# Optimization experiments

Measured on AMD Instinct MI355X. Metric: run time of the kernel, lower is better.

## Reference

```python
import jax, jax.numpy as jnp
import numpy as np

EMBED = 1024
HEADS = 16
HEAD_DIM = EMBED // HEADS
MLP = 4 * EMBED
EPS = 1e-6


def setup_inputs() -> dict:
    key = jax.random.key(0)
    ks = jax.random.split(key, 16)
    B, N, C = 2, 2048, EMBED
    x = jax.random.normal(ks[0], (B, N, C), dtype=jnp.float32)
    c = jax.random.normal(ks[1], (B, C), dtype=jnp.float32)
    attention_mask = jax.random.randint(ks[2], (B, N), 0, 2, dtype=jnp.int32)
    s = 0.02
    params = {
        "norm_w": jnp.ones((C,), jnp.float32),
        "scale_w": s * jax.random.normal(ks[3], (C, C), jnp.float32),
        "scale_b": s * jax.random.normal(ks[4], (C,), jnp.float32),
        "shift_w": s * jax.random.normal(ks[5], (C, C), jnp.float32),
        "shift_b": s * jax.random.normal(ks[6], (C,), jnp.float32),
        "qkv_w": s * jax.random.normal(ks[7], (3 * C, C), jnp.float32),
        "proj_w": s * jax.random.normal(ks[8], (C, C), jnp.float32),
        "proj_b": s * jax.random.normal(ks[9], (C,), jnp.float32),
        "mlp_w1": s * jax.random.normal(ks[10], (2 * MLP, C), jnp.float32),
        "mlp_b1": s * jax.random.normal(ks[11], (2 * MLP,), jnp.float32),
        "mlp_w2": s * jax.random.normal(ks[12], (C, MLP), jnp.float32),
        "mlp_b2": s * jax.random.normal(ks[13], (C,), jnp.float32),
    }
    return {"x": x, "c": c, "attention_mask": attention_mask, **params}


def _adaln(x, c, norm_w, scale_w, scale_b, shift_w, shift_b):
    sc = jax.nn.silu(c)
    shift = sc @ shift_w.T + shift_b                      # [B,C]
    scale = jnp.clip(sc @ scale_w.T + scale_b + 1.0, 0.1, 10.0)
    # RMSNorm: ||x|| * C^-0.5, clamped below by eps
    norm = jnp.maximum(jnp.linalg.norm(x, axis=-1, keepdims=True) * x.shape[-1] ** -0.5, EPS)
    h = x / norm * norm_w
    return h * scale[:, None, :] + shift[:, None, :]


def _attention(x, attention_mask, qkv_w, proj_w, proj_b):
    B, N, C = x.shape
    qkv = (x @ qkv_w.T).reshape(B, N, 3, HEADS, HEAD_DIM)
    q = qkv[:, :, 0].transpose(0, 2, 1, 3)  # [B,H,N,D]
    k = qkv[:, :, 1].transpose(0, 2, 1, 3)
    v = qkv[:, :, 2].transpose(0, 2, 1, 3)
    attn = jnp.einsum("bhnd,bhmd->bhnm", q, k) * (HEAD_DIM ** -0.5)
    mask = attention_mask[:, None, None, :]              # [B,1,1,N] over keys
    attn = jnp.where(mask == 0, -jnp.inf, attn)
    all_inf = jnp.all(attn == -jnp.inf, axis=-1, keepdims=True)
    attn = jnp.where(all_inf, 0.0, attn)
    p = jax.nn.softmax(attn, axis=-1)
    out = jnp.einsum("bhnm,bhmd->bhnd", p, v).transpose(0, 2, 1, 3).reshape(B, N, C)
    return out @ proj_w.T + proj_b


def _mlp(x, w1, b1, w2, b2):
    h = x @ w1.T + b1
    x1, x2 = jnp.split(h, 2, axis=-1)
    return (jax.nn.silu(x1) * x2) @ w2.T + b2


def reference(x, c, attention_mask, norm_w, scale_w, scale_b, shift_w, shift_b,
              qkv_w, proj_w, proj_b, mlp_w1, mlp_b1, mlp_w2, mlp_b2):
    x = x + _attention(_adaln(x, c, norm_w, scale_w, scale_b, shift_w, shift_b),
                       attention_mask, qkv_w, proj_w, proj_b)
    x = x + _mlp(_adaln(x, c, norm_w, scale_w, scale_b, shift_w, shift_b),
                 mlp_w1, mlp_b1, mlp_w2, mlp_b2)
    return x
```

## Files before the change

### kernel.cpp

```cpp
#include <hip/hip_runtime.h>
#include <cstdint>
#include <cstddef>

#define DEVINL __device__ __forceinline__

typedef __bf16 bf16x8 __attribute__((ext_vector_type(8)));
typedef float  f32x4  __attribute__((ext_vector_type(4)));


DEVINL unsigned short f2b(float f) {
  unsigned u = __builtin_bit_cast(unsigned, f);
  u += 0x7fffu + ((u >> 16) & 1u);
  return (unsigned short)(u >> 16);
}

DEVINL unsigned packtrunc(float a, float b) {
  unsigned ua = __builtin_bit_cast(unsigned, a);
  unsigned ub = __builtin_bit_cast(unsigned, b);
  return (ua >> 16) | (ub & 0xffff0000u);
}

DEVINL void async16(void* lds, const void* g) {
  __builtin_amdgcn_global_load_lds((const __attribute__((address_space(1))) unsigned*)g,
                                   (__attribute__((address_space(3))) unsigned*)lds,
                                   16, 0, 0);
}


__global__ void cvt4_kernel(const float* __restrict__ s0, const float* __restrict__ s1,
                            const float* __restrict__ s2, const float* __restrict__ s3,
                            unsigned short* __restrict__ d0, unsigned short* __restrict__ d1,
                            unsigned short* __restrict__ d2, unsigned short* __restrict__ d3) {
  int i = blockIdx.x * 256 + threadIdx.x;
  if (i < 786432) {
    float4 v = ((const float4*)s0)[i];
    ushort4 o; o.x = f2b(v.x); o.y = f2b(v.y); o.z = f2b(v.z); o.w = f2b(v.w);
    ((ushort4*)d0)[i] = o;
  } else if (i < 1048576) {
    int off = i - 786432;
    float4 v = ((const float4*)s1)[off];
    ushort4 o; o.x = f2b(v.x); o.y = f2b(v.y); o.z = f2b(v.z); o.w = f2b(v.w);
    ((ushort4*)d1)[off] = o;
  } else if (i < 3145728) {
    int off = i - 1048576;
    int row = off >> 8, col = off & 255;
    int rp = (row < 4096) ? (row << 1) : (((row - 4096) << 1) | 1);
    float4 v = ((const float4*)s2)[off];
    ushort4 o; o.x = f2b(v.x); o.y = f2b(v.y); o.z = f2b(v.z); o.w = f2b(v.w);
    ((ushort4*)d2)[rp * 256 + col] = o;
  } else {
    int off = i - 3145728;
    float4 v = ((const float4*)s3)[off];
    ushort4 o; o.x = f2b(v.x); o.y = f2b(v.y); o.z = f2b(v.z); o.w = f2b(v.w);
    ((ushort4*)d3)[off] = o;
  }
}


__global__ void cond_kernel(const float* __restrict__ c,
                            const float* __restrict__ scale_w, const float* __restrict__ scale_b,
                            const float* __restrict__ shift_w, const float* __restrict__ shift_b,
                            float* __restrict__ scale_o, float* __restrict__ shift_o) {
  __shared__ float sc[1024];
  __shared__ float red[2][4][64];
  int tid = threadIdx.x;
  int b = blockIdx.x >> 4, ch = blockIdx.x & 15;
  for (int i = tid; i < 1024; i += 256) {
    float cv = c[b * 1024 + i];
    sc[i] = cv / (1.f + __expf(-cv));
  }
  __syncthreads();
  int colidx = tid & 63, p = tid >> 6;
  int co = ch * 64 + colidx;
  float dsc = 0.f, dsh = 0.f;
  for (int i = 0; i < 256; ++i) {
    int kk = p * 256 + i;
    float s = sc[kk];
    dsc += s * scale_w[(size_t)co * 1024 + kk];
    dsh += s * shift_w[(size_t)co * 1024 + kk];
  }
  red[0][p][colidx] = dsc;
  red[1][p][colidx] = dsh;
  __syncthreads();
  if (p == 0) {
    float s4  = red[0][0][colidx] + red[0][1][colidx] + red[0][2][colidx] + red[0][3][colidx];
    float sh4 = red[1][0][colidx] + red[1][1][colidx] + red[1][2][colidx] + red[1][3][colidx];
    scale_o[b * 1024 + co] = fminf(fmaxf(s4 + scale_b[co] + 1.f, 0.1f), 10.f);
    shift_o[b * 1024 + co] = sh4 + shift_b[co];
  }
}


__global__ __launch_bounds__(256) void adaln_kernel(const float* __restrict__ x,
                                                    const float* __restrict__ norm_w,
                                                    const float* __restrict__ scale,
                                                    const float* __restrict__ shift,
                                                    unsigned short* __restrict__ h) {
  int row = blockIdx.x;
  int b = row >> 11;
  int tid = threadIdx.x;
  float4 v = ((const float4*)(x + (size_t)row * 1024))[tid];
  float ss = v.x * v.x + v.y * v.y + v.z * v.z + v.w * v.w;
  #pragma unroll
  for (int d = 32; d; d >>= 1) ss += __shfl_xor(ss, d);
  __shared__ float wsum[4];
  if ((tid & 63) == 0) wsum[tid >> 6] = ss;
  __syncthreads();
  float tot = wsum[0] + wsum[1] + wsum[2] + wsum[3];
  float inv = 1.f / fmaxf(sqrtf(tot * (1.f / 1024.f)), 1e-6f);
  float4 nw  = ((const float4*)norm_w)[tid];
  float4 scv = ((const float4*)(scale + b * 1024))[tid];
  float4 shv = ((const float4*)(shift + b * 1024))[tid];
  ushort4 o;
  o.x = f2b(v.x * inv * nw.x * scv.x + shv.x);
  o.y = f2b(v.y * inv * nw.y * scv.y + shv.y);
  o.z = f2b(v.z * inv * nw.z * scv.z + shv.z);
  o.w = f2b(v.w * inv * nw.w * scv.w + shv.w);
  ((ushort4*)(h + (size_t)row * 1024))[tid] = o;
}


template<int EPI, int MT>
__global__ __launch_bounds__(256, 1) void gemm_k(
    const unsigned short* __restrict__ A,
    const unsigned short* __restrict__ B0,
    const float* __restrict__ bias0,
    const float* __restrict__ resid,
    void* __restrict__ out0_, void* __restrict__ out1_, void* __restrict__ out2_,
    int M, int N, int K) {
  constexpr int MI = MT / 32;
  constexpr int A_SH = MT * 32;
  constexpr int COMPUTE_SH = 2 * A_SH + 2 * 4096;
  constexpr int STAGE_SH = (EPI == 1) ? 128 * 136 : (EPI == 2 ? 128 * 72 : 0);
  constexpr int SMEM_SH = (COMPUTE_SH > STAGE_SH) ? COMPUTE_SH : STAGE_SH;
  __shared__ __align__(16) unsigned short smem[SMEM_SH];
  unsigned short* As0 = smem;
  unsigned short* As1 = smem + A_SH;
  unsigned short* Bs0 = smem + 2 * A_SH;
  unsigned short* Bs1 = smem + 2 * A_SH + 4096;

  const int tid = threadIdx.x;
  const int wave = tid >> 6, lane = tid & 63;
  const int quad = lane >> 4, l16 = lane & 15;
  const int wm = (wave >> 1) * (MT / 2), wn = (wave & 1) * 64;
  const int bm = blockIdx.y * MT, bn = blockIdx.x * 128;

  f32x4 acc[MI][4] = {};

  const int steps = K >> 6;
  for (int s = 0; s < steps; ++s) {
    const int k0 = s << 6;
    __syncthreads();
    #pragma unroll
    for (int i = 0; i < MT / 64; ++i) {
      int cc = i * 256 + tid;
      int r = cc >> 2, ko = (cc & 3) << 3;
      size_t ga = (size_t)(bm + r) * K + k0 + ko;
      async16(As0 + (i * 2048 + wave * 512), A + ga);
      async16(As1 + (i * 2048 + wave * 512), A + ga + 32);
    }
    #pragma unroll
    for (int i = 0; i < 2; ++i) {
      int cc = i * 256 + tid;
      int r = cc >> 2, ko = (cc & 3) << 3;
      size_t gb = (size_t)(bn + r) * K + k0 + ko;
      async16(Bs0 + (i * 2048 + wave * 512), B0 + gb);
      async16(Bs1 + (i * 2048 + wave * 512), B0 + gb + 32);
    }
    __syncthreads();
    #pragma unroll
    for (int ks = 0; ks < 2; ++ks) {
      const unsigned short* Ah = ks ? As1 : As0;
      const unsigned short* Bh = ks ? Bs1 : Bs0;
      bf16x8 af[MI], bfr[4];
      #pragma unroll
      for (int mi = 0; mi < MI; ++mi)
        af[mi] = *reinterpret_cast<const bf16x8*>(&Ah[(wm + mi * 16 + l16) * 32 + quad * 8]);
      #pragma unroll
      for (int ni = 0; ni < 4; ++ni)
        bfr[ni] = *reinterpret_cast<const bf16x8*>(&Bh[(wn + ni * 16 + l16) * 32 + quad * 8]);
      #pragma unroll
      for (int mi = 0; mi < MI; ++mi)
        #pragma unroll
        for (int ni = 0; ni < 4; ++ni)
          acc[mi][ni] = __builtin_amdgcn_mfma_f32_16x16x32_bf16(af[mi], bfr[ni], acc[mi][ni], 0, 0, 0);
    }
  }

  if constexpr (EPI == 0) {
    #pragma unroll
    for (int mi = 0; mi < MI; ++mi) {
      #pragma unroll
      for (int ni = 0; ni < 4; ++ni) {
        int gc = bn + wn + ni * 16 + l16;
        #pragma unroll
        for (int r = 0; r < 4; ++r) {
          int gr = bm + wm + mi * 16 + quad * 4 + r;
          ((float*)out0_)[(size_t)gr * N + gc] = acc[mi][ni][r] + bias0[gc] + resid[(size_t)gr * N + gc];
        }
      }
    }
  } else if constexpr (EPI == 1) {
    const int region = bn >> 10;
    __syncthreads();
    #pragma unroll
    for (int mi = 0; mi < MI; ++mi) {
      #pragma unroll
      for (int ni = 0; ni < 4; ++ni) {
        int lc = wn + ni * 16 + l16;
        #pragma unroll
        for (int r = 0; r < 4; ++r) {
          int lr = wm + mi * 16 + quad * 4 + r;
          float v = acc[mi][ni][r];
          if (region == 0)      smem[lr * 136 + lc] = f2b(v * 0.125f);
          else if (region == 1) smem[lr * 136 + lc] = f2b(v);
          else                  smem[lc * 136 + lr] = f2b(v);
        }
      }
    }
    __syncthreads();
    const int b = bm >> 11;
    const int bnm = bn & 1023;
    if (region <= 1) {
      int lr = tid >> 1, hl = tid & 1;
      int n = (bm + lr) & 2047;
      int hh = (bnm >> 6) + hl;
      unsigned short* dst = (unsigned short*)(region == 0 ? out0_ : out1_) +
                            (((size_t)(b * 16 + hh)) * 2048 + n) * 64;
      const unsigned short* src = smem + lr * 136 + hl * 64;
      #pragma unroll
      for (int j = 0; j < 8; ++j)
        ((uint4*)dst)[j] = *(const uint4*)(src + j * 8);
    } else {
      int lc = tid >> 1, nh = tid & 1;
      int c2 = bnm + lc;
      int hh = c2 >> 6, d = c2 & 63;
      int nbase = (bm & 2047) + nh * 64;
      unsigned short* dst = (unsigned short*)out2_ +
                            (((size_t)(b * 16 + hh)) * 64 + d) * 2048 + nbase;
      const unsigned short* src = smem + lc * 136 + nh * 64;
      #pragma unroll
      for (int j = 0; j < 8; ++j)
        ((uint4*)dst)[j] = *(const uint4*)(src + j * 8);
    }
  } else {
    __syncthreads();
    #pragma unroll
    for (int mi = 0; mi < MI; ++mi) {
      #pragma unroll
      for (int ni = 0; ni < 4; ++ni) {
        int lc = wn + ni * 16 + l16;
        int gcp = bn + lc;
        int gi = gcp >> 1;
        float bias = bias0[(gcp & 1) ? 4096 + gi : gi];
        #pragma unroll
        for (int r = 0; r < 4; ++r) {
          int lr = wm + mi * 16 + quad * 4 + r;
          float v = acc[mi][ni][r] + bias;
          float p = __shfl_xor(v, 1);
          if ((l16 & 1) == 0) {
            float g = (v / (1.f + __expf(-v))) * p;
            smem[lr * 72 + (lc >> 1)] = f2b(g);
          }
        }
      }
    }
    __syncthreads();
    int lr = tid >> 1, ch = (tid & 1) * 32;
    unsigned short* dst = (unsigned short*)out0_ + (size_t)(bm + lr) * (N >> 1) + (bn >> 1) + ch;
    const unsigned short* src = smem + lr * 72 + ch;
    #pragma unroll
    for (int j = 0; j < 4; ++j)
      ((uint4*)dst)[j] = *(const uint4*)(src + j * 8);
  }
}


__global__ __launch_bounds__(512, 1) void attn_kernel(
    const unsigned short* __restrict__ q, const unsigned short* __restrict__ k,
    const unsigned short* __restrict__ vt, const int* __restrict__ amask,
    unsigned short* __restrict__ o) {
  const int bh = blockIdx.x;
  const int b = bh >> 4, h = bh & 15;
  const int qt = blockIdx.y;
  const int tid = threadIdx.x;
  const int wave = tid >> 6, lane = tid & 63;
  const int quad = lane >> 4, l16 = lane & 15;
  const int h7 = l16 & 7;
  const int kc0 = (quad ^ h7) * 8;
  const int kc1 = ((quad + 4) ^ h7) * 8;

  const unsigned short* qb = q  + (size_t)bh * 2048 * 64;
  const unsigned short* kb = k  + (size_t)bh * 2048 * 64;
  const unsigned short* vb = vt + (size_t)bh * 64 * 2048;

  __shared__ __align__(16) unsigned short Ks[64 * 64];
  __shared__ __align__(16) unsigned short Vs[64 * 64];
  __shared__ __align__(16) unsigned short Ps[8 * 16 * 72];
  __shared__ float biasf[64];

  unsigned short* PsW = Ps + wave * 1152;

  const int qrow = qt * 128 + wave * 16 + l16;
  bf16x8 qa0 = *reinterpret_cast<const bf16x8*>(&qb[(size_t)qrow * 64 + quad * 8]);
  bf16x8 qa1 = *reinterpret_cast<const bf16x8*>(&qb[(size_t)qrow * 64 + 32 + quad * 8]);

  f32x4 oacc[4] = {};
  float mrow = -30000.f, lrow = 0.f;

  uint4 kpre, vpre;
  {
    int key = tid >> 3, dl = (tid & 7) ^ (key & 7);
    kpre = *(const uint4*)(kb + key * 64 + dl * 8);
    int d = tid >> 3, kl = (tid & 7) ^ (d & 7);
    vpre = *(const uint4*)(vb + (size_t)d * 2048 + kl * 8);
  }
  int mv = (tid < 64) ? amask[b * 2048 + tid] : 0;

  for (int kt = 0; kt < 32; ++kt) {
    __syncthreads();
    ((uint4*)Ks)[tid] = kpre;
    ((uint4*)Vs)[tid] = vpre;
    if (tid < 64) biasf[tid] = mv ? 0.f : -30000.f;
    __syncthreads();

    if (kt + 1 < 32) {
      int key = tid >> 3, dl = (tid & 7) ^ (key & 7);
      kpre = *(const uint4*)(kb + (size_t)(kt + 1) * 4096 + key * 64 + dl * 8);
      int d = tid >> 3, kl = (tid & 7) ^ (d & 7);
      vpre = *(const uint4*)(vb + (size_t)d * 2048 + (kt + 1) * 64 + kl * 8);
      mv = (tid < 64) ? amask[b * 2048 + (kt + 1) * 64 + tid] : 0;
    }

    f32x4 st[4];
    #pragma unroll
    for (int nt = 0; nt < 4; ++nt) {
      bf16x8 ka0 = *reinterpret_cast<const bf16x8*>(&Ks[(nt * 16 + l16) * 64 + kc0]);
      bf16x8 ka1 = *reinterpret_cast<const bf16x8*>(&Ks[(nt * 16 + l16) * 64 + kc1]);
      f32x4 bv = *reinterpret_cast<const f32x4*>(&biasf[nt * 16 + quad * 4]);
      f32x4 z = {};
      z = __builtin_amdgcn_mfma_f32_16x16x32_bf16(ka0, qa0, z, 0, 0, 0);
      z = __builtin_amdgcn_mfma_f32_16x16x32_bf16(ka1, qa1, z, 0, 0, 0);
      st[nt] = z + bv;
    }

    float tm = -1e30f;
    #pragma unroll
    for (int nt = 0; nt < 4; ++nt)
      #pragma unroll
      for (int r = 0; r < 4; ++r) tm = fmaxf(tm, st[nt][r]);
    tm = fmaxf(tm, __shfl_xor(tm, 16));
    tm = fmaxf(tm, __shfl_xor(tm, 32));

    float mnew = fmaxf(mrow, tm);
    float alpha = __expf(mrow - mnew);
    mrow = mnew;

    float rs = 0.f;
    #pragma unroll
    for (int nt = 0; nt < 4; ++nt) {
      float p0 = __expf(st[nt][0] - mnew);
      float p1 = __expf(st[nt][1] - mnew);
      float p2 = __expf(st[nt][2] - mnew);
      float p3 = __expf(st[nt][3] - mnew);
      rs += (p0 + p1) + (p2 + p3);
      uint2 w;
      w.x = packtrunc(p0, p1);
      w.y = packtrunc(p2, p3);
      *(uint2*)&PsW[l16 * 72 + nt * 16 + quad * 4] = w;
    }
    rs += __shfl_xor(rs, 16);
    rs += __shfl_xor(rs, 32);
    lrow = lrow * alpha + rs;

    float a0 = __shfl(alpha, quad * 4 + 0);
    float a1 = __shfl(alpha, quad * 4 + 1);
    float a2 = __shfl(alpha, quad * 4 + 2);
    float a3 = __shfl(alpha, quad * 4 + 3);
    #pragma unroll
    for (int dt = 0; dt < 4; ++dt) {
      oacc[dt][0] *= a0; oacc[dt][1] *= a1; oacc[dt][2] *= a2; oacc[dt][3] *= a3;
    }

    bf16x8 pa0 = *reinterpret_cast<const bf16x8*>(&PsW[l16 * 72 + quad * 8]);
    bf16x8 pa1 = *reinterpret_cast<const bf16x8*>(&PsW[l16 * 72 + 32 + quad * 8]);
    #pragma unroll
    for (int dt = 0; dt < 4; ++dt) {
      bf16x8 vb0 = *reinterpret_cast<const bf16x8*>(&Vs[(dt * 16 + l16) * 64 + kc0]);
      bf16x8 vb1 = *reinterpret_cast<const bf16x8*>(&Vs[(dt * 16 + l16) * 64 + kc1]);
      oacc[dt] = __builtin_amdgcn_mfma_f32_16x16x32_bf16(pa0, vb0, oacc[dt], 0, 0, 0);
      oacc[dt] = __builtin_amdgcn_mfma_f32_16x16x32_bf16(pa1, vb1, oacc[dt], 0, 0, 0);
    }
  }

  float invl = lrow > 0.f ? 1.f / lrow : 0.f;
  float i0 = __shfl(invl, quad * 4 + 0);
  float i1 = __shfl(invl, quad * 4 + 1);
  float i2 = __shfl(invl, quad * 4 + 2);
  float i3 = __shfl(invl, quad * 4 + 3);
  __syncthreads();
  #pragma unroll
  for (int dt = 0; dt < 4; ++dt) {
    int lr = wave * 16 + quad * 4;
    Ps[(lr + 0) * 72 + dt * 16 + l16] = f2b(oacc[dt][0] * i0);
    Ps[(lr + 1) * 72 + dt * 16 + l16] = f2b(oacc[dt][1] * i1);
    Ps[(lr + 2) * 72 + dt * 16 + l16] = f2b(oacc[dt][2] * i2);
    Ps[(lr + 3) * 72 + dt * 16 + l16] = f2b(oacc[dt][3] * i3);
  }
  __syncthreads();
  {
    int lr = tid >> 2, cb = (tid & 3) * 16;
    int n = qt * 128 + lr;
    unsigned short* dst = o + ((size_t)(b * 2048 + n)) * 1024 + h * 64 + cb;
    const unsigned short* src = Ps + lr * 72 + cb;
    ((uint4*)dst)[0] = *(const uint4*)(src);
    ((uint4*)dst)[1] = *(const uint4*)(src + 8);
  }
}


extern "C" void kernel_launch(void* const* d_in, const int* in_sizes, int n_in,
                              void* d_out, int out_size, void* d_ws, size_t ws_size,
                              hipStream_t stream) {
  const float* x       = (const float*)d_in[0];
  const float* c       = (const float*)d_in[1];
  const int*   amask   = (const int*)d_in[2];
  const float* norm_w  = (const float*)d_in[3];
  const float* scale_w = (const float*)d_in[4];
  const float* scale_b = (const float*)d_in[5];
  const float* shift_w = (const float*)d_in[6];
  const float* shift_b = (const float*)d_in[7];
  const float* qkv_w   = (const float*)d_in[8];
  const float* proj_w  = (const float*)d_in[9];
  const float* proj_b  = (const float*)d_in[10];
  const float* mlp_w1  = (const float*)d_in[11];
  const float* mlp_b1  = (const float*)d_in[12];
  const float* mlp_w2  = (const float*)d_in[13];
  const float* mlp_b2  = (const float*)d_in[14];

  char* ws = (char*)d_ws;
  unsigned short* wqkv  = (unsigned short*)(ws + 0);
  unsigned short* wproj = (unsigned short*)(ws + 6291456);
  unsigned short* wmlp1 = (unsigned short*)(ws + 8388608);
  unsigned short* wmlp2 = (unsigned short*)(ws + 25165824);
  float* scale_o        = (float*)(ws + 33554432);
  float* shift_o        = (float*)(ws + 33562624);
  unsigned short* hbuf  = (unsigned short*)(ws + 33570816);
  unsigned short* qbuf  = (unsigned short*)(ws + 41959424);
  unsigned short* kbuf  = (unsigned short*)(ws + 50348032);
  unsigned short* vbuf  = (unsigned short*)(ws + 58736640);
  unsigned short* abuf  = (unsigned short*)(ws + 67125248);
  unsigned short* gbuf  = qbuf;
  float* x1             = (float*)(ws + 75513856);

  cvt4_kernel<<<16384, 256, 0, stream>>>(qkv_w, proj_w, mlp_w1, mlp_w2,
                                         wqkv, wproj, wmlp1, wmlp2);

  cond_kernel<<<32, 256, 0, stream>>>(c, scale_w, scale_b, shift_w, shift_b, scale_o, shift_o);

  adaln_kernel<<<4096, 256, 0, stream>>>(x, norm_w, scale_o, shift_o, hbuf);

  gemm_k<1, 128><<<dim3(24, 32), 256, 0, stream>>>(hbuf, wqkv, nullptr, nullptr,
                                                   qbuf, kbuf, vbuf, 4096, 3072, 1024);

  attn_kernel<<<dim3(32, 16), 512, 0, stream>>>(qbuf, kbuf, vbuf, amask, abuf);

  gemm_k<0, 64><<<dim3(8, 64), 256, 0, stream>>>(abuf, wproj, proj_b, x,
                                                 x1, nullptr, nullptr, 4096, 1024, 1024);

  adaln_kernel<<<4096, 256, 0, stream>>>(x1, norm_w, scale_o, shift_o, hbuf);

  gemm_k<2, 128><<<dim3(64, 32), 256, 0, stream>>>(hbuf, wmlp1, mlp_b1, nullptr,
                                                   gbuf, nullptr, nullptr, 4096, 8192, 1024);

  gemm_k<0, 64><<<dim3(8, 64), 256, 0, stream>>>(gbuf, wmlp2, mlp_b2, x1,
                                                 d_out, nullptr, nullptr, 4096, 1024, 4096);

  (void)in_sizes; (void)n_in; (void)out_size; (void)ws_size;
}
```

Before: 468.0 us.

## Add 256x256-tile GLU GEMM kernel for MLP up-projection

```diff
diff --git a/kernel.cpp b/kernel.cpp
--- a/kernel.cpp
+++ b/kernel.cpp
@@ -276,6 +276,129 @@
 }
 
 
+__global__ __launch_bounds__(512, 2) void gemm256_glu(
+    const unsigned short* __restrict__ A,
+    const unsigned short* __restrict__ B,
+    const float* __restrict__ bias,
+    unsigned short* __restrict__ out,
+    int M, int N, int K) {
+  __shared__ __align__(16) unsigned short smem[65536];
+
+  const int tid  = threadIdx.x;
+  const int wave = tid >> 6, lane = tid & 63;
+  const int quad = lane >> 4, l16 = lane & 15;
+  const int wm = (wave >> 2) * 128, wn = (wave & 3) * 64;
+
+  const int nwg = gridDim.x * gridDim.y;
+  int lin = blockIdx.y * gridDim.x + blockIdx.x;
+  int cpx = nwg >> 3;
+  int swz = (lin & 7) * cpx + (lin >> 3);
+  int bx = swz % gridDim.x, by = swz / gridDim.x;
+  const int bm = by * 256, bn = bx * 256;
+
+  const unsigned short* gA[4];
+  const unsigned short* gB[4];
+  #pragma unroll
+  for (int j = 0; j < 4; ++j) {
+    int cc = j * 512 + tid;
+    int r  = cc >> 3;
+    int lc = (cc & 7) ^ (r & 7);
+    gA[j] = A + (size_t)(bm + r) * K + lc * 8;
+    gB[j] = B + (size_t)(bn + r) * K + lc * 8;
+  }
+
+  f32x4 acc[8][4] = {};
+  const int T = K >> 6;
+
+  #pragma unroll
+  for (int j = 0; j < 4; ++j) async16(smem +         j * 4096 + wave * 512, gA[j]);
+  #pragma unroll
+  for (int j = 0; j < 4; ++j) async16(smem + 32768 + j * 4096 + wave * 512, gB[j]);
+  #pragma unroll
+  for (int j = 0; j < 4; ++j) async16(smem + 16384 + j * 4096 + wave * 512, gA[j] + 64);
+  #pragma unroll
+  for (int j = 0; j < 4; ++j) async16(smem + 49152 + j * 4096 + wave * 512, gB[j] + 64);
+  asm volatile("s_waitcnt vmcnt(8)" ::: "memory");
+  __builtin_amdgcn_s_barrier();
+
+  const int pc0 = quad ^ (l16 & 7);
+  const int pc1 = (quad + 4) ^ (l16 & 7);
+
+  for (int t = 0; t < T; ++t) {
+    const int cur = t & 1;
+    const unsigned short* As = smem + cur * 16384;
+    const unsigned short* Bs = smem + 32768 + cur * 16384;
+
+    bf16x8 bfr[4][2];
+    #pragma unroll
+    for (int ni = 0; ni < 4; ++ni) {
+      int rb = (wn + ni * 16 + l16) * 64;
+      bfr[ni][0] = *reinterpret_cast<const bf16x8*>(&Bs[rb + pc0 * 8]);
+      bfr[ni][1] = *reinterpret_cast<const bf16x8*>(&Bs[rb + pc1 * 8]);
+    }
+    __builtin_amdgcn_s_setprio(1);
+    #pragma unroll
+    for (int mi = 0; mi < 8; ++mi) {
+      int ra = (wm + mi * 16 + l16) * 64;
+      bf16x8 a0 = *reinterpret_cast<const bf16x8*>(&As[ra + pc0 * 8]);
+      bf16x8 a1 = *reinterpret_cast<const bf16x8*>(&As[ra + pc1 * 8]);
+      #pragma unroll
+      for (int ni = 0; ni < 4; ++ni)
+        acc[mi][ni] = __builtin_amdgcn_mfma_f32_16x16x32_bf16(a0, bfr[ni][0], acc[mi][ni], 0, 0, 0);
+      #pragma unroll
+      for (int ni = 0; ni < 4; ++ni)
+        acc[mi][ni] = __builtin_amdgcn_mfma_f32_16x16x32_bf16(a1, bfr[ni][1], acc[mi][ni], 0, 0, 0);
+    }
+    __builtin_amdgcn_s_setprio(0);
+
+    asm volatile("s_waitcnt lgkmcnt(0)" ::: "memory");
+    __builtin_amdgcn_s_barrier();
+
+    if (t + 2 < T) {
+      const int ko = (t + 2) << 6;
+      #pragma unroll
+      for (int j = 0; j < 4; ++j) async16(smem + cur * 16384 +         j * 4096 + wave * 512, gA[j] + ko);
+      #pragma unroll
+      for (int j = 0; j < 4; ++j) async16(smem + cur * 16384 + 32768 + j * 4096 + wave * 512, gB[j] + ko);
+      asm volatile("s_waitcnt vmcnt(8)" ::: "memory");
+      __builtin_amdgcn_s_barrier();
+    } else if (t + 1 < T) {
+      asm volatile("s_waitcnt vmcnt(0)" ::: "memory");
+      __builtin_amdgcn_s_barrier();
+    }
+  }
+
+  #pragma unroll
+  for (int ni = 0; ni < 4; ++ni) {
+    int lc = wn + ni * 16 + l16;
+    int gi = (bn + lc) >> 1;
+    float bv = bias[(l16 & 1) ? 4096 + gi : gi];
+    #pragma unroll
+    for (int mi = 0; mi < 8; ++mi) {
+      #pragma unroll
+      for (int r = 0; r < 4; ++r) {
+        float v = acc[mi][ni][r] + bv;
+        float p = __shfl_xor(v, 1);
+        if ((l16 & 1) == 0) {
+          int lr = wm + mi * 16 + quad * 4 + r;
+          float g = (v / (1.f + __expf(-v))) * p;
+          smem[lr * 136 + (lc >> 1)] = f2b(g);
+        }
+      }
+    }
+  }
+  __syncthreads();
+  {
+    int lr = tid >> 1, half = (tid & 1) * 64;
+    unsigned short* dst = out + (size_t)(bm + lr) * (N >> 1) + (bn >> 1) + half;
+    const unsigned short* src = smem + lr * 136 + half;
+    #pragma unroll
+    for (int j = 0; j < 8; ++j)
+      ((uint4*)dst)[j] = *(const uint4*)(src + j * 8);
+  }
+}
+
+
 __global__ __launch_bounds__(512, 1) void attn_kernel(
     const unsigned short* __restrict__ q, const unsigned short* __restrict__ k,
     const unsigned short* __restrict__ vt, const int* __restrict__ amask,
@@ -470,8 +593,7 @@
 
   adaln_kernel<<<4096, 256, 0, stream>>>(x1, norm_w, scale_o, shift_o, hbuf);
 
-  gemm_k<2, 128><<<dim3(64, 32), 256, 0, stream>>>(hbuf, wmlp1, mlp_b1, nullptr,
-                                                   gbuf, nullptr, nullptr, 4096, 8192, 1024);
+  gemm256_glu<<<dim3(32, 16), 512, 0, stream>>>(hbuf, wmlp1, mlp_b1, gbuf, 4096, 8192, 1024);
 
   gemm_k<0, 64><<<dim3(8, 64), 256, 0, stream>>>(gbuf, wmlp2, mlp_b2, x1,
                                                  d_out, nullptr, nullptr, 4096, 1024, 4096);
```

New measurement: 482.2 us. 3.0% more time.

## Add 256x256-tile 8-wave GEMM with fused SwiGLU epilogue for MLP up-projection

Applied to the files above, without the earlier changes.

```diff
diff --git a/kernel.cpp b/kernel.cpp
--- a/kernel.cpp
+++ b/kernel.cpp
@@ -276,6 +276,153 @@
 }
 
 
+__global__ __launch_bounds__(512, 2) void gemm256_glu(
+    const unsigned short* __restrict__ A,
+    const unsigned short* __restrict__ B,
+    const float* __restrict__ bias,
+    unsigned short* __restrict__ out,
+    int M, int N, int K) {
+  __shared__ __align__(16) unsigned short smem[65536];
+
+  const int tid  = threadIdx.x;
+  const int wave = tid >> 6, lane = tid & 63;
+  const int quad = lane >> 4, l16 = lane & 15;
+  const int wm = (wave >> 2) * 128, wn = (wave & 3) * 64;
+
+  const int nwg = gridDim.x * gridDim.y;
+  int lin = blockIdx.y * gridDim.x + blockIdx.x;
+  int cpx = nwg >> 3;
+  int swz = (lin & 7) * cpx + (lin >> 3);
+  int bx = swz % gridDim.x, by = swz / gridDim.x;
+  const int bm = by * 256, bn = bx * 256;
+
+  const int srow = tid >> 3;
+  const int slc  = (tid & 7) ^ (srow & 7);
+  const unsigned short* gA0 = A + (size_t)(bm + srow) * K + slc * 8;
+  const unsigned short* gB0 = B + (size_t)(bn + srow) * K + slc * 8;
+  const size_t rstep = (size_t)64 * K;
+
+#define STAGE_A(h, tk, d) do { \
+    const unsigned short* s_ = gA0 + (size_t)(h) * 128 * K + (size_t)(tk) * 64; \
+    async16(smem + (d) * 16384 + (h) * 8192 + tid * 8, s_); \
+    async16(smem + (d) * 16384 + (h) * 8192 + 4096 + tid * 8, s_ + rstep); \
+  } while (0)
+#define STAGE_B(h, tk, d) do { \
+    const unsigned short* s_ = gB0 + (size_t)(h) * 128 * K + (size_t)(tk) * 64; \
+    async16(smem + 32768 + (d) * 16384 + (h) * 8192 + tid * 8, s_); \
+    async16(smem + 32768 + (d) * 16384 + (h) * 8192 + 4096 + tid * 8, s_ + rstep); \
+  } while (0)
+
+  const int pc0 = (quad ^ (l16 & 7)) * 8;
+  const int pc1 = ((quad + 4) ^ (l16 & 7)) * 8;
+  const int arow = wm + l16;
+  const int brow = wn + l16;
+
+  f32x4 acc[8][4] = {};
+  bf16x8 bfr[4][2];
+  const int T = K >> 6;
+  const int JI = T >> 1;
+
+  STAGE_B(0, 0, 0); STAGE_B(1, 0, 0);
+  STAGE_A(0, 0, 0); STAGE_A(1, 0, 0);
+  STAGE_B(0, 1, 1); STAGE_B(1, 1, 1);
+  asm volatile("s_waitcnt vmcnt(4)" ::: "memory");
+  __builtin_amdgcn_s_barrier();
+
+#define READ_BFR(d) do { \
+    _Pragma("unroll") \
+    for (int ni = 0; ni < 4; ++ni) { \
+      int rb = 32768 + (d) * 16384 + (brow + ni * 16) * 64; \
+      bfr[ni][0] = *reinterpret_cast<const bf16x8*>(&smem[rb + pc0]); \
+      bfr[ni][1] = *reinterpret_cast<const bf16x8*>(&smem[rb + pc1]); \
+    } \
+  } while (0)
+
+#define PHASE(d, q, RB, STAGE_STMT, TAIL_STMT) do { \
+    bf16x8 a00, a01, a10, a11; \
+    if (RB) READ_BFR(d); \
+    { int ra = (d) * 16384 + (arow + (2 * (q)) * 16) * 64; \
+      a00 = *reinterpret_cast<const bf16x8*>(&smem[ra + pc0]); \
+      a01 = *reinterpret_cast<const bf16x8*>(&smem[ra + pc1]); \
+      a10 = *reinterpret_cast<const bf16x8*>(&smem[ra + 1024 + pc0]); \
+      a11 = *reinterpret_cast<const bf16x8*>(&smem[ra + 1024 + pc1]); } \
+    STAGE_STMT; \
+    if (RB) asm volatile("s_waitcnt lgkmcnt(8)" ::: "memory"); \
+    __builtin_amdgcn_s_barrier(); \
+    asm volatile("s_waitcnt lgkmcnt(0)" ::: "memory"); \
+    __builtin_amdgcn_sched_barrier(0); \
+    __builtin_amdgcn_s_setprio(1); \
+    _Pragma("unroll") \
+    for (int ni = 0; ni < 4; ++ni) \
+      acc[2 * (q)][ni] = __builtin_amdgcn_mfma_f32_16x16x32_bf16(a00, bfr[ni][0], acc[2 * (q)][ni], 0, 0, 0); \
+    _Pragma("unroll") \
+    for (int ni = 0; ni < 4; ++ni) \
+      acc[2 * (q) + 1][ni] = __builtin_amdgcn_mfma_f32_16x16x32_bf16(a10, bfr[ni][0], acc[2 * (q) + 1][ni], 0, 0, 0); \
+    _Pragma("unroll") \
+    for (int ni = 0; ni < 4; ++ni) \
+      acc[2 * (q)][ni] = __builtin_amdgcn_mfma_f32_16x16x32_bf16(a01, bfr[ni][1], acc[2 * (q)][ni], 0, 0, 0); \
+    _Pragma("unroll") \
+    for (int ni = 0; ni < 4; ++ni) \
+      acc[2 * (q) + 1][ni] = __builtin_amdgcn_mfma_f32_16x16x32_bf16(a11, bfr[ni][1], acc[2 * (q) + 1][ni], 0, 0, 0); \
+    __builtin_amdgcn_s_setprio(0); \
+    TAIL_STMT; \
+    __builtin_amdgcn_s_barrier(); \
+  } while (0)
+
+  for (int j = 0; j < JI; ++j) {
+    const int t1 = 2 * j + 1, t2 = 2 * j + 2, t3 = 2 * j + 3;
+    const bool g2 = (t2 < T), g3 = (t3 < T);
+    PHASE(0, 0, 1, { STAGE_A(0, t1, 1); }, {});
+    PHASE(0, 1, 0, { STAGE_A(1, t1, 1); }, {});
+    PHASE(0, 2, 0, { if (g2) STAGE_B(0, t2, 0); }, {});
+    PHASE(0, 3, 0, { if (g2) STAGE_B(1, t2, 0); },
+          { if (g2) { asm volatile("s_waitcnt vmcnt(4)" ::: "memory"); }
+            else    { asm volatile("s_waitcnt vmcnt(0)" ::: "memory"); } });
+    PHASE(1, 0, 1, { if (g2) STAGE_A(0, t2, 0); }, {});
+    PHASE(1, 1, 0, { if (g2) STAGE_A(1, t2, 0); }, {});
+    PHASE(1, 2, 0, { if (g3) STAGE_B(0, t3, 1); }, {});
+    PHASE(1, 3, 0, { if (g3) STAGE_B(1, t3, 1); },
+          { if (j + 1 < JI) {
+              if (g3) { asm volatile("s_waitcnt vmcnt(4)" ::: "memory"); }
+              else    { asm volatile("s_waitcnt vmcnt(0)" ::: "memory"); } } });
+  }
+
+#undef PHASE
+#undef READ_BFR
+#undef STAGE_A
+#undef STAGE_B
+
+  #pragma unroll
+  for (int ni = 0; ni < 4; ++ni) {
+    int lc = wn + ni * 16 + l16;
+    int gi = (bn + lc) >> 1;
+    float bv = bias[(l16 & 1) ? 4096 + gi : gi];
+    #pragma unroll
+    for (int mi = 0; mi < 8; ++mi) {
+      #pragma unroll
+      for (int r = 0; r < 4; ++r) {
+        float v = acc[mi][ni][r] + bv;
+        float p = __shfl_xor(v, 1);
+        if ((l16 & 1) == 0) {
+          int lr = wm + mi * 16 + quad * 4 + r;
+          float g = (v / (1.f + __expf(-v))) * p;
+          smem[lr * 136 + (lc >> 1)] = f2b(g);
+        }
+      }
+    }
+  }
+  __syncthreads();
+  {
+    int lr = tid >> 1, half = (tid & 1) * 64;
+    unsigned short* dst = out + (size_t)(bm + lr) * (N >> 1) + (bn >> 1) + half;
+    const unsigned short* src = smem + lr * 136 + half;
+    #pragma unroll
+    for (int j = 0; j < 8; ++j)
+      ((uint4*)dst)[j] = *(const uint4*)(src + j * 8);
+  }
+}
+
+
 __global__ __launch_bounds__(512, 1) void attn_kernel(
     const unsigned short* __restrict__ q, const unsigned short* __restrict__ k,
     const unsigned short* __restrict__ vt, const int* __restrict__ amask,
@@ -470,8 +617,7 @@
 
   adaln_kernel<<<4096, 256, 0, stream>>>(x1, norm_w, scale_o, shift_o, hbuf);
 
-  gemm_k<2, 128><<<dim3(64, 32), 256, 0, stream>>>(hbuf, wmlp1, mlp_b1, nullptr,
-                                                   gbuf, nullptr, nullptr, 4096, 8192, 1024);
+  gemm256_glu<<<dim3(32, 16), 512, 0, stream>>>(hbuf, wmlp1, mlp_b1, gbuf, 4096, 8192, 1024);
 
   gemm_k<0, 64><<<dim3(8, 64), 256, 0, stream>>>(gbuf, wmlp2, mlp_b2, x1,
                                                  d_out, nullptr, nullptr, 4096, 1024, 4096);
```

Result: no change. 476.9 us (+1.9%).
